# Performance work log

Hardware: AMD Instinct MI355X
Metric: run time of the kernel (lower is better)

## Reference

```python
import jax, jax.numpy as jnp
import numpy as np
from jax import lax

B, N, CIN, COUT, R, K = 4, 16384, 64, 128, 32, 3
VOX_EPS = 1e-6
BN3D_EPS = 1e-4
BN1D_EPS = 1e-5
LRELU_SLOPE = 0.1


def setup_inputs() -> dict:
    key = jax.random.key(0)
    ks = jax.random.split(key, 20)
    d = {}
    d['features'] = jax.random.normal(ks[0], (B, N, CIN), jnp.float32)
    d['coords'] = jax.random.normal(ks[1], (B, N, 3), jnp.float32)
    # Conv3D #1: (D,H,W,Cin,Cout) + bias
    d['conv1_w'] = jax.random.normal(ks[2], (K, K, K, CIN, COUT), jnp.float32) * 0.02
    d['conv1_b'] = jax.random.normal(ks[3], (COUT,), jnp.float32) * 0.02
    d['bn1_g'] = jax.random.uniform(ks[4], (COUT,), jnp.float32, 0.75, 1.25)
    d['bn1_b'] = jax.random.normal(ks[5], (COUT,), jnp.float32) * 0.1
    d['bn1_m'] = jax.random.normal(ks[6], (COUT,), jnp.float32) * 0.1
    d['bn1_v'] = jax.random.uniform(ks[7], (COUT,), jnp.float32, 0.5, 1.5)
    # Conv3D #2
    d['conv2_w'] = jax.random.normal(ks[8], (K, K, K, COUT, COUT), jnp.float32) * 0.02
    d['conv2_b'] = jax.random.normal(ks[9], (COUT,), jnp.float32) * 0.02
    d['bn2_g'] = jax.random.uniform(ks[10], (COUT,), jnp.float32, 0.75, 1.25)
    d['bn2_b'] = jax.random.normal(ks[11], (COUT,), jnp.float32) * 0.1
    d['bn2_m'] = jax.random.normal(ks[12], (COUT,), jnp.float32) * 0.1
    d['bn2_v'] = jax.random.uniform(ks[13], (COUT,), jnp.float32, 0.5, 1.5)
    # Point SharedMLP: Conv1D k=1 -> matmul, + BN + ReLU
    d['pw'] = jax.random.normal(ks[14], (CIN, COUT), jnp.float32) * 0.05
    d['pb'] = jax.random.normal(ks[15], (COUT,), jnp.float32) * 0.02
    d['pbn_g'] = jax.random.uniform(ks[16], (COUT,), jnp.float32, 0.75, 1.25)
    d['pbn_b'] = jax.random.normal(ks[17], (COUT,), jnp.float32) * 0.1
    d['pbn_m'] = jax.random.normal(ks[18], (COUT,), jnp.float32) * 0.1
    d['pbn_v'] = jax.random.uniform(ks[19], (COUT,), jnp.float32, 0.5, 1.5)
    return d


def _bn(x, g, b, m, v, eps):
    return (x - m) * (g * lax.rsqrt(v + eps)) + b


def _leaky_relu(x):
    return jnp.where(x >= 0, x, LRELU_SLOPE * x)


def _pvconv(features, coords, conv1_w, conv1_b, bn1_g, bn1_b, bn1_m, bn1_v,
            conv2_w, conv2_b, bn2_g, bn2_b, bn2_m, bn2_v,
            pw, pb, pbn_g, pbn_b, pbn_m, pbn_v):
    r = R
    # ---- Voxelization (normalize coords, scatter-average into grid) ----
    c = lax.stop_gradient(coords)                                   # (B,N,3)
    nc = c - jnp.mean(c, axis=1, keepdims=True)
    denom = jnp.max(jnp.linalg.norm(nc, axis=2, keepdims=True), axis=1, keepdims=True) * 2.0 + VOX_EPS
    nc = nc / denom + 0.5
    nc = jnp.clip(nc * r, 0.0, r - 1)                                # (B,N,3) in [0, r-1]
    vox = jnp.round(nc).astype(jnp.int32)                            # (B,N,3)

    batch_off = jnp.arange(B, dtype=jnp.int32)[:, None] * (r * r * r)
    lin = batch_off + vox[..., 0] * (r * r) + vox[..., 1] * r + vox[..., 2]  # (B,N)
    lin = lin.reshape(-1)
    feat_flat = features.reshape(-1, CIN)
    sums = jax.ops.segment_sum(feat_flat, lin, num_segments=B * r * r * r)   # (B*r^3,Cin)
    cnts = jax.ops.segment_sum(jnp.ones((B * N,), jnp.float32), lin, num_segments=B * r * r * r)
    cnts = jnp.where(cnts == 0, 1.0, cnts)
    grid = (sums / cnts[:, None]).reshape(B, r, r, r, CIN)           # (B,r,r,r,Cin)

    # ---- Voxel branch: Conv3D -> BN -> LeakyReLU (x2) ----
    dn = ('NDHWC', 'DHWIO', 'NDHWC')
    g = lax.conv_general_dilated(grid, conv1_w, (1, 1, 1), 'SAME', dimension_numbers=dn) + conv1_b
    g = _leaky_relu(_bn(g, bn1_g, bn1_b, bn1_m, bn1_v, BN3D_EPS))
    g = lax.conv_general_dilated(g, conv2_w, (1, 1, 1), 'SAME', dimension_numbers=dn) + conv2_b
    g = _leaky_relu(_bn(g, bn2_g, bn2_b, bn2_m, bn2_v, BN3D_EPS))    # (B,r,r,r,Cout)

    # ---- Trilinear devoxelize: gather 8 corners with interpolation weights ----
    g_flat = g.reshape(B, r * r * r, COUT)
    c0 = jnp.floor(nc).astype(jnp.int32)                             # (B,N,3)
    frac = nc - c0.astype(nc.dtype)
    c1 = jnp.minimum(c0 + 1, r - 1)
    vox_pts = jnp.zeros((B, N, COUT), jnp.float32)
    for dx in (0, 1):
        for dy in (0, 1):
            for dz in (0, 1):
                ix = c1[..., 0] if dx else c0[..., 0]
                iy = c1[..., 1] if dy else c0[..., 1]
                iz = c1[..., 2] if dz else c0[..., 2]
                w = ((frac[..., 0] if dx else 1.0 - frac[..., 0]) *
                     (frac[..., 1] if dy else 1.0 - frac[..., 1]) *
                     (frac[..., 2] if dz else 1.0 - frac[..., 2]))   # (B,N)
                idx = ix * (r * r) + iy * r + iz                      # (B,N)
                gathered = jnp.take_along_axis(g_flat, idx[..., None], axis=1)  # (B,N,Cout)
                vox_pts = vox_pts + w[..., None] * gathered

    # ---- Point branch: SharedMLP (1x1 conv -> BN -> ReLU) ----
    pf = jnp.einsum('bnc,cd->bnd', features, pw) + pb
    pf = jax.nn.relu(_bn(pf, pbn_g, pbn_b, pbn_m, pbn_v, BN1D_EPS))

    return vox_pts + pf                                              # (B,N,Cout)


def reference(features, coords, conv1_w, conv1_b, bn1_g, bn1_b, bn1_m, bn1_v,
              conv2_w, conv2_b, bn2_g, bn2_b, bn2_m, bn2_v,
              pw, pb, pbn_g, pbn_b, pbn_m, pbn_v):
    fused = _pvconv(features, coords, conv1_w, conv1_b, bn1_g, bn1_b, bn1_m, bn1_v,
                    conv2_w, conv2_b, bn2_g, bn2_b, bn2_m, bn2_v,
                    pw, pb, pbn_g, pbn_b, pbn_m, pbn_v)
    return (fused, coords)
```

## Files before the change

kernel.cpp:

```cpp
#include <hip/hip_runtime.h>
#include <hip/hip_bf16.h>

constexpr int B    = 4;
constexpr int N    = 16384;
constexpr int CIN  = 64;
constexpr int COUT = 128;
constexpr int R    = 32;
constexpr int R3   = R * R * R;
constexpr int RP   = 34;
constexpr int RP3  = RP * RP * RP;
constexpr int NVOX = B * R3;
constexpr float VOX_EPS   = 1e-6f;
constexpr float BN3D_EPS  = 1e-4f;
constexpr float BN1D_EPS  = 1e-5f;
constexpr float LRELU     = 0.1f;

typedef __attribute__((ext_vector_type(8))) short bf16x8;
typedef __attribute__((ext_vector_type(4))) float f32x4;
typedef __attribute__((ext_vector_type(8))) unsigned short u16x8;

__device__ inline float bf2f(ushort u) {
    union { unsigned int i; float f; } x; x.i = ((unsigned int)u) << 16; return x.f;
}
__device__ inline ushort f2bf(float f) {
    union { float f; unsigned int i; } x; x.f = f;
    unsigned int r = x.i + 0x7fffu + ((x.i >> 16) & 1u);
    return (ushort)(r >> 16);
}

__device__ inline int swz(int base, int z) {
    return (base ^ (z & 3) ^ ((z >> 2) & 3)) & 3;
}

__global__ __launch_bounds__(256) void k_stats_sum(const float* __restrict__ coords,
                                                   float* __restrict__ stats) {
    int blk = blockIdx.x;
    int b = blk >> 4, stripe = blk & 15;
    const float* c = coords + ((size_t)b * N + stripe * 1024) * 3;
    float sx = 0.f, sy = 0.f, sz = 0.f;
    for (int i = threadIdx.x; i < 1024; i += 256) {
        sx += c[i * 3 + 0];
        sy += c[i * 3 + 1];
        sz += c[i * 3 + 2];
    }
    __shared__ float red[256];
    float vals[3] = {sx, sy, sz};
    for (int k = 0; k < 3; ++k) {
        red[threadIdx.x] = vals[k];
        __syncthreads();
        for (int s = 128; s > 0; s >>= 1) {
            if (threadIdx.x < s) red[threadIdx.x] += red[threadIdx.x + s];
            __syncthreads();
        }
        if (threadIdx.x == 0) atomicAdd(&stats[b * 8 + k], red[0]);
        __syncthreads();
    }
}

__global__ __launch_bounds__(256) void k_stats_max(const float* __restrict__ coords,
                                                   float* __restrict__ stats) {
    int blk = blockIdx.x;
    int b = blk >> 4, stripe = blk & 15;
    const float invN = 1.0f / (float)N;
    float mx = stats[b * 8 + 0] * invN;
    float my = stats[b * 8 + 1] * invN;
    float mz = stats[b * 8 + 2] * invN;
    const float* c = coords + ((size_t)b * N + stripe * 1024) * 3;
    float mm = 0.f;
    for (int i = threadIdx.x; i < 1024; i += 256) {
        float dx = c[i * 3 + 0] - mx;
        float dy = c[i * 3 + 1] - my;
        float dz = c[i * 3 + 2] - mz;
        mm = fmaxf(mm, sqrtf(dx * dx + dy * dy + dz * dz));
    }
    __shared__ float red[256];
    red[threadIdx.x] = mm;
    __syncthreads();
    for (int s = 128; s > 0; s >>= 1) {
        if (threadIdx.x < s) red[threadIdx.x] = fmaxf(red[threadIdx.x], red[threadIdx.x + s]);
        __syncthreads();
    }
    if (threadIdx.x == 0)
        atomicMax((unsigned*)&stats[b * 8 + 3], __float_as_uint(red[0]));
}

__device__ inline void compute_nc(const float* __restrict__ coords,
                                  const float* __restrict__ stats,
                                  int p, int b, float& nx, float& ny, float& nz) {
    const float invN = 1.0f / (float)N;
    float mmax = __uint_as_float(((const unsigned*)stats)[b * 8 + 3]);
    float denom = mmax * 2.0f + VOX_EPS;
    float cx = coords[(size_t)p * 3 + 0];
    float cy = coords[(size_t)p * 3 + 1];
    float cz = coords[(size_t)p * 3 + 2];
    nx = (cx - stats[b * 8 + 0] * invN) / denom + 0.5f;
    ny = (cy - stats[b * 8 + 1] * invN) / denom + 0.5f;
    nz = (cz - stats[b * 8 + 2] * invN) / denom + 0.5f;
    nx = fminf(fmaxf(nx * (float)R, 0.f), (float)(R - 1));
    ny = fminf(fmaxf(ny * (float)R, 0.f), (float)(R - 1));
    nz = fminf(fmaxf(nz * (float)R, 0.f), (float)(R - 1));
}

__global__ __launch_bounds__(256) void k_count(const float* __restrict__ coords,
                                               const float* __restrict__ stats,
                                               int* __restrict__ cnt,
                                               int* __restrict__ plin,
                                               int* __restrict__ pslot) {
    int p = blockIdx.x * 256 + threadIdx.x;
    int b = p >> 14;
    float nx, ny, nz;
    compute_nc(coords, stats, p, b, nx, ny, nz);
    int lin = ((b * R + (int)rintf(nx)) * R + (int)rintf(ny)) * R + (int)rintf(nz);
    plin[p] = lin;
    pslot[p] = atomicAdd(&cnt[lin], 1);
}

__global__ __launch_bounds__(256) void k_scan1(const int* __restrict__ cnt,
                                               int* __restrict__ base,
                                               int* __restrict__ btot) {
    __shared__ int s[256];
    int g = blockIdx.x * 256 + threadIdx.x;
    int val = cnt[g];
    s[threadIdx.x] = val;
    __syncthreads();
    for (int off = 1; off < 256; off <<= 1) {
        int v = threadIdx.x >= off ? s[threadIdx.x - off] : 0;
        __syncthreads();
        s[threadIdx.x] += v;
        __syncthreads();
    }
    base[g] = s[threadIdx.x] - val;
    if (threadIdx.x == 255) btot[blockIdx.x] = s[255];
}

__global__ __launch_bounds__(512) void k_scan2(const int* __restrict__ btot,
                                               int* __restrict__ boff) {
    __shared__ int s[512];
    int val = btot[threadIdx.x];
    s[threadIdx.x] = val;
    __syncthreads();
    for (int off = 1; off < 512; off <<= 1) {
        int v = threadIdx.x >= off ? s[threadIdx.x - off] : 0;
        __syncthreads();
        s[threadIdx.x] += v;
        __syncthreads();
    }
    boff[threadIdx.x] = s[threadIdx.x] - val;
}

__global__ __launch_bounds__(256) void k_fill(const int* __restrict__ plin,
                                              const int* __restrict__ pslot,
                                              const int* __restrict__ base,
                                              const int* __restrict__ boff,
                                              int* __restrict__ order) {
    int p = blockIdx.x * 256 + threadIdx.x;
    int lin = plin[p];
    order[base[lin] + boff[lin >> 8] + pslot[p]] = p;
}

__global__ __launch_bounds__(256) void k_gather(const float* __restrict__ feats,
                                                const int* __restrict__ cnt,
                                                const int* __restrict__ base,
                                                const int* __restrict__ boff,
                                                const int* __restrict__ order,
                                                ushort* __restrict__ gridp) {
    int v = blockIdx.x * 4 + (threadIdx.x >> 6);
    int lane = threadIdx.x & 63;
    int c = cnt[v];
    int bs = base[v] + boff[v >> 8];
    float acc = 0.f;
    for (int j = 0; j < c; ++j) {
        int p = order[bs + j];
        acc += feats[(size_t)p * CIN + lane];
    }
    float val = acc / (float)(c == 0 ? 1 : c);
    int vz = v & 31, vy = (v >> 5) & 31, vx = (v >> 10) & 31, b = v >> 15;
    size_t o = ((((size_t)(b * 2 + (lane >> 5)) * RP + vx + 1) * RP + vy + 1) * RP + (vz + 1)) * 32
               + (lane & 31);
    gridp[o] = f2bf(val);
}

__global__ __launch_bounds__(256) void k_zero_border(ushort* __restrict__ buf, int nchunks) {
    int i = blockIdx.x * 256 + threadIdx.x;
    if (i >= nchunks) return;
    int v = i >> 2;
    int r = v % RP3;
    int z = r % RP;
    int t = r / RP;
    int y = t % RP;
    int x = (t / RP) % RP;
    if (x == 0 || x == RP - 1 || y == 0 || y == RP - 1 || z == 0 || z == RP - 1)
        *(uint4*)(buf + (size_t)i * 8) = make_uint4(0u, 0u, 0u, 0u);
}

__global__ __launch_bounds__(256) void k_wq_all(const float* __restrict__ w1,
                                                const float* __restrict__ w2,
                                                const float* __restrict__ pw,
                                                ushort* __restrict__ wq) {
    int idx = blockIdx.x * 256 + threadIdx.x;
    int g = idx >> 12;
    const float* src; int gl;
    if (g < 54)       { src = w1; gl = g; }
    else if (g < 162) { src = w2; gl = g - 54; }
    else              { src = pw; gl = g - 162; }
    int j    = idx & 7;
    int lane = (idx >> 3) & 63;
    int nt   = (idx >> 9) & 7;
    int k = gl * 32 + ((lane >> 4) << 3) + j;
    int n = nt * 16 + (lane & 15);
    wq[idx] = f2bf(src[(size_t)k * COUT + n]);
}

template <int CI, bool PLANAR_OUT>
__global__ __launch_bounds__(256, 3) void k_conv_mfma(const ushort* __restrict__ in,
                                                      const ushort* __restrict__ wq,
                                                      const float* __restrict__ bias,
                                                      const float* __restrict__ bng,
                                                      const float* __restrict__ bnb,
                                                      const float* __restrict__ bnm,
                                                      const float* __restrict__ bnv,
                                                      ushort* __restrict__ out) {
    constexpr int NCHI = CI / 32;
    __shared__ __align__(16) ushort sl[18 * RP * 32];

    int bid = blockIdx.x;
    int Y = bid & 7;
    int x = (bid >> 3) & 31;
    int b = bid >> 8;
    int y0 = Y * 4;
    int tid = threadIdx.x;
    int wave = tid >> 6, lane = tid & 63, quad = lane >> 4, l16 = lane & 15;
    int wm = wave >> 1, wn = wave & 1;

    f32x4 acc[4][4] = {};

    for (int cc = 0; cc < NCHI; ++cc) {
        const ushort* base = in + (((size_t)(b * NCHI + cc) * RP + x) * RP + y0) * RP * 32;
        __syncthreads();
        for (int t = tid; t < 18 * 136; t += 256) {
            int row = t / 136;
            int r   = t - row * 136;
            int X = row / 6, Yl = row - X * 6;
            uint4 v = *(const uint4*)(base + ((size_t)(X * RP + Yl) * RP) * 32 + r * 8);
            int z = r >> 2, ch = r & 3;
            *(uint4*)(sl + ((row * RP + z) * 4 + swz(ch, z)) * 8) = v;
        }
        __syncthreads();

        for (int tap = 0; tap < 27; ++tap) {
            int dx = tap / 9, rem = tap - dx * 9;
            int dy = rem / 3, dz = rem - dy * 3;

            const ushort* bp = wq + ((size_t)((tap * NCHI + cc) * 8 + wn * 4) * 64 + lane) * 8;
            bf16x8 bfr[4], afr[4];
#pragma unroll
            for (int nt = 0; nt < 4; ++nt)
                bfr[nt] = *(const bf16x8*)(bp + nt * 512);
#pragma unroll
            for (int mt = 0; mt < 4; ++mt) {
                int row18 = dx * 6 + wm * 2 + (mt >> 1) + dy;
                int zrow = ((mt & 1) << 4) + l16 + dz;
                afr[mt] = *(const bf16x8*)(sl + ((row18 * RP + zrow) * 4 + swz(quad, zrow)) * 8);
            }
#pragma unroll
            for (int mt = 0; mt < 4; ++mt)
#pragma unroll
                for (int nt = 0; nt < 4; ++nt)
                    acc[mt][nt] = __builtin_amdgcn_mfma_f32_16x16x32_bf16(
                        afr[mt], bfr[nt], acc[mt][nt], 0, 0, 0);
        }
    }

    float sc[4], sb[4], bs[4];
#pragma unroll
    for (int nt = 0; nt < 4; ++nt) {
        int co = wn * 64 + nt * 16 + l16;
        sc[nt] = bng[co] * rsqrtf(bnv[co] + BN3D_EPS);
        sb[nt] = bnb[co] - bnm[co] * sc[nt];
        bs[nt] = bias[co];
    }
#pragma unroll
    for (int mt = 0; mt < 4; ++mt) {
#pragma unroll
        for (int reg = 0; reg < 4; ++reg) {
            int m = wm * 64 + mt * 16 + quad * 4 + reg;
            int i = m >> 5, z = m & 31;
#pragma unroll
            for (int nt = 0; nt < 4; ++nt) {
                float v = (acc[mt][nt][reg] + bs[nt]) * sc[nt] + sb[nt];
                v = v >= 0.f ? v : LRELU * v;
                int co = wn * 64 + nt * 16 + l16;
                if (PLANAR_OUT) {
                    size_t o = ((((size_t)(b * 4 + (co >> 5)) * RP + (x + 1)) * RP
                                 + (y0 + i + 1)) * RP + (z + 1)) * 32 + (co & 31);
                    out[o] = f2bf(v);
                } else {
                    size_t o = (((size_t)(b * R + x) * R + (y0 + i)) * R + z) * COUT + co;
                    out[o] = f2bf(v);
                }
            }
        }
    }
}

__global__ __launch_bounds__(256, 2) void k_devox(const float* __restrict__ coords,
                                                  const float* __restrict__ feats,
                                                  const float* __restrict__ stats,
                                                  const ushort* __restrict__ g2,
                                                  const ushort* __restrict__ pwq,
                                                  const float* __restrict__ pb,
                                                  const float* __restrict__ pg,
                                                  const float* __restrict__ pbb,
                                                  const float* __restrict__ pm,
                                                  const float* __restrict__ pv,
                                                  float* __restrict__ out) {
    __shared__ __align__(16) ushort sfeat[128 * 64];
    __shared__ __align__(16) ushort smlp[128 * 128];
    __shared__ int   sidx[128 * 8];
    __shared__ float swt[128 * 8];

    int blk = blockIdx.x, tid = threadIdx.x;
    int wave = tid >> 6, lane = tid & 63, quad = lane >> 4, l16 = lane & 15;
    int p0 = blk * 128;

    if (tid < 128) {
        int p = p0 + tid, b = p >> 14;
        float nx, ny, nz;
        compute_nc(coords, stats, p, b, nx, ny, nz);
        int cx0 = (int)floorf(nx), cy0 = (int)floorf(ny), cz0 = (int)floorf(nz);
        float fx = nx - (float)cx0, fy = ny - (float)cy0, fz = nz - (float)cz0;
        int cx1 = min(cx0 + 1, R - 1), cy1 = min(cy0 + 1, R - 1), cz1 = min(cz0 + 1, R - 1);
#pragma unroll
        for (int k = 0; k < 8; ++k) {
            int dx = (k >> 2) & 1, dy = (k >> 1) & 1, dz = k & 1;
            int ix = dx ? cx1 : cx0;
            int iy = dy ? cy1 : cy0;
            int iz = dz ? cz1 : cz0;
            sidx[tid * 8 + k] = (((b * R + ix) * R + iy) * R + iz) * COUT;
            swt[tid * 8 + k] = (dx ? fx : 1.f - fx) * (dy ? fy : 1.f - fy) * (dz ? fz : 1.f - fz);
        }
    }
    for (int i = 0; i < 4; ++i) {
        int c = i * 256 + tid;
        int p = c >> 3, ch = c & 7;
        const float* src = feats + (size_t)(p0 + p) * CIN + ch * 8;
        float4 f0 = *(const float4*)src;
        float4 f1 = *(const float4*)(src + 4);
        u16x8 u;
        u[0] = f2bf(f0.x); u[1] = f2bf(f0.y); u[2] = f2bf(f0.z); u[3] = f2bf(f0.w);
        u[4] = f2bf(f1.x); u[5] = f2bf(f1.y); u[6] = f2bf(f1.z); u[7] = f2bf(f1.w);
        *(u16x8*)&sfeat[(p * 8 + (ch ^ (p & 7))) * 8] = u;
    }
    __syncthreads();

    f32x4 acc[8][2] = {};
#pragma unroll
    for (int cc = 0; cc < 2; ++cc) {
        const ushort* bp = pwq + ((size_t)(cc * 8 + wave * 2) * 64 + lane) * 8;
        bf16x8 b0 = *(const bf16x8*)bp;
        bf16x8 b1 = *(const bf16x8*)(bp + 512);
#pragma unroll
        for (int mt = 0; mt < 8; ++mt) {
            int prow = mt * 16 + l16;
            int ch = cc * 4 + quad;
            bf16x8 a = *(const bf16x8*)&sfeat[(prow * 8 + (ch ^ (prow & 7))) * 8];
            acc[mt][0] = __builtin_amdgcn_mfma_f32_16x16x32_bf16(a, b0, acc[mt][0], 0, 0, 0);
            acc[mt][1] = __builtin_amdgcn_mfma_f32_16x16x32_bf16(a, b1, acc[mt][1], 0, 0, 0);
        }
    }

    int co0 = wave * 32 + l16, co1 = co0 + 16;
    {
        float sc0 = pg[co0] * rsqrtf(pv[co0] + BN1D_EPS);
        float sb0 = pbb[co0] - pm[co0] * sc0;
        float bs0 = pb[co0];
        float sc1 = pg[co1] * rsqrtf(pv[co1] + BN1D_EPS);
        float sb1 = pbb[co1] - pm[co1] * sc1;
        float bs1 = pb[co1];
#pragma unroll
        for (int mt = 0; mt < 8; ++mt) {
#pragma unroll
            for (int reg = 0; reg < 4; ++reg) {
                int pl = mt * 16 + quad * 4 + reg;
                smlp[pl * 128 + co0] = f2bf(fmaxf((acc[mt][0][reg] + bs0) * sc0 + sb0, 0.f));
                smlp[pl * 128 + co1] = f2bf(fmaxf((acc[mt][1][reg] + bs1) * sc1 + sb1, 0.f));
            }
        }
    }
    __syncthreads();

#pragma unroll
    for (int it = 0; it < 8; ++it) {
        int t = it * 256 + tid;
        int p = t >> 4, c = t & 15;
        float a[8];
        const ushort* m = &smlp[p * 128 + c * 8];
#pragma unroll
        for (int j = 0; j < 8; ++j) a[j] = bf2f(m[j]);
#pragma unroll
        for (int k = 0; k < 8; ++k) {
            int idx = sidx[p * 8 + k];
            float w = swt[p * 8 + k];
            bf16x8 row = *(const bf16x8*)(g2 + (size_t)idx + c * 8);
#pragma unroll
            for (int j = 0; j < 8; ++j) a[j] += w * bf2f(((u16x8)row)[j]);
        }
        float* o = out + (size_t)(p0 + p) * COUT + c * 8;
        *(float4*)o       = make_float4(a[0], a[1], a[2], a[3]);
        *(float4*)(o + 4) = make_float4(a[4], a[5], a[6], a[7]);
    }
}

extern "C" void kernel_launch(void* const* d_in, const int* in_sizes, int n_in,
                              void* d_out, int out_size, void* d_ws, size_t ws_size,
                              hipStream_t stream) {
    const float* feats   = (const float*)d_in[0];
    const float* coords  = (const float*)d_in[1];
    const float* conv1_w = (const float*)d_in[2];
    const float* conv1_b = (const float*)d_in[3];
    const float* bn1_g   = (const float*)d_in[4];
    const float* bn1_b   = (const float*)d_in[5];
    const float* bn1_m   = (const float*)d_in[6];
    const float* bn1_v   = (const float*)d_in[7];
    const float* conv2_w = (const float*)d_in[8];
    const float* conv2_b = (const float*)d_in[9];
    const float* bn2_g   = (const float*)d_in[10];
    const float* bn2_b   = (const float*)d_in[11];
    const float* bn2_m   = (const float*)d_in[12];
    const float* bn2_v   = (const float*)d_in[13];
    const float* pw      = (const float*)d_in[14];
    const float* pb      = (const float*)d_in[15];
    const float* pbn_g   = (const float*)d_in[16];
    const float* pbn_b   = (const float*)d_in[17];
    const float* pbn_m   = (const float*)d_in[18];
    const float* pbn_v   = (const float*)d_in[19];

    char* p = (char*)d_ws;
    float* stats = (float*)p;                        p += 256;
    int*   cnt   = (int*)p;                          p += (size_t)NVOX * 4;
    int*   plin  = (int*)p;                          p += (size_t)B * N * 4;
    int*   pslot = (int*)p;                          p += (size_t)B * N * 4;
    int*   base  = (int*)p;                          p += (size_t)NVOX * 4;
    int*   btot  = (int*)p;                          p += 512 * 4;
    int*   boff  = (int*)p;                          p += 512 * 4;
    int*   order = (int*)p;                          p += (size_t)B * N * 4;
    ushort* gridp = (ushort*)p;                      p += (size_t)B * 2 * RP3 * 32 * 2;
    ushort* g1p   = (ushort*)p;                      p += (size_t)B * 4 * RP3 * 32 * 2;
    ushort* g2b   = (ushort*)p;                      p += (size_t)B * R3 * COUT * 2;
    ushort* wq    = (ushort*)p;                      p += (size_t)164 * 4096 * 2;
    ushort* wq1 = wq;
    ushort* wq2 = wq + 54 * 4096;
    ushort* pwq = wq + 162 * 4096;
    float*  outf  = (float*)d_out;

    hipMemsetAsync(stats, 0, 256 + (size_t)NVOX * 4, stream);
    {
        int nc = B * 6 * RP3 * 4;
        k_zero_border<<<(nc + 255) / 256, 256, 0, stream>>>(gridp, nc);
    }

    k_stats_sum<<<64, 256, 0, stream>>>(coords, stats);
    k_stats_max<<<64, 256, 0, stream>>>(coords, stats);

    k_count<<<(B * N) / 256, 256, 0, stream>>>(coords, stats, cnt, plin, pslot);
    k_scan1<<<NVOX / 256, 256, 0, stream>>>(cnt, base, btot);
    k_scan2<<<1, 512, 0, stream>>>(btot, boff);
    k_fill<<<(B * N) / 256, 256, 0, stream>>>(plin, pslot, base, boff, order);
    k_gather<<<NVOX / 4, 256, 0, stream>>>(feats, cnt, base, boff, order, gridp);

    k_wq_all<<<(164 * 4096) / 256, 256, 0, stream>>>(conv1_w, conv2_w, pw, wq);

    k_conv_mfma<CIN, true><<<B * R * (R / 4), 256, 0, stream>>>(
        gridp, wq1, conv1_b, bn1_g, bn1_b, bn1_m, bn1_v, g1p);
    k_conv_mfma<COUT, false><<<B * R * (R / 4), 256, 0, stream>>>(
        g1p, wq2, conv2_b, bn2_g, bn2_b, bn2_m, bn2_v, g2b);

    k_devox<<<(B * N) / 128, 256, 0, stream>>>(coords, feats, stats, g2b, pwq, pb,
                                               pbn_g, pbn_b, pbn_m, pbn_v, outf);

    hipMemcpyAsync(outf + (size_t)B * N * COUT, coords, (size_t)B * N * 3 * sizeof(float),
                   hipMemcpyDeviceToDevice, stream);
}
```

Before: 354.1 us.

## Fuse voxelization preprocessing into one persistent kernel with grid barriers

Merges the stats, count, scan, fill, gather, border-zeroing and weight-quantization kernels into a single 256-block persistent kernel that uses atomic grid-wide barriers between phases. The coords copy moves from a separate memcpy into the tail of the devox kernel. This removes about ten kernel launches and their gaps. In exchange the gather phase now runs on only 256 blocks instead of 8192, which lowers parallelism. The spin barriers also assume all blocks are co-resident.

```diff
diff --git a/kernel.cpp b/kernel.cpp
--- a/kernel.cpp
+++ b/kernel.cpp
@@ -32,56 +32,15 @@
     return (base ^ (z & 3) ^ ((z >> 2) & 3)) & 3;
 }
 
-__global__ __launch_bounds__(256) void k_stats_sum(const float* __restrict__ coords,
-                                                   float* __restrict__ stats) {
-    int blk = blockIdx.x;
-    int b = blk >> 4, stripe = blk & 15;
-    const float* c = coords + ((size_t)b * N + stripe * 1024) * 3;
-    float sx = 0.f, sy = 0.f, sz = 0.f;
-    for (int i = threadIdx.x; i < 1024; i += 256) {
-        sx += c[i * 3 + 0];
-        sy += c[i * 3 + 1];
-        sz += c[i * 3 + 2];
-    }
-    __shared__ float red[256];
-    float vals[3] = {sx, sy, sz};
-    for (int k = 0; k < 3; ++k) {
-        red[threadIdx.x] = vals[k];
-        __syncthreads();
-        for (int s = 128; s > 0; s >>= 1) {
-            if (threadIdx.x < s) red[threadIdx.x] += red[threadIdx.x + s];
-            __syncthreads();
-        }
-        if (threadIdx.x == 0) atomicAdd(&stats[b * 8 + k], red[0]);
-        __syncthreads();
-    }
-}
-
-__global__ __launch_bounds__(256) void k_stats_max(const float* __restrict__ coords,
-                                                   float* __restrict__ stats) {
-    int blk = blockIdx.x;
-    int b = blk >> 4, stripe = blk & 15;
-    const float invN = 1.0f / (float)N;
-    float mx = stats[b * 8 + 0] * invN;
-    float my = stats[b * 8 + 1] * invN;
-    float mz = stats[b * 8 + 2] * invN;
-    const float* c = coords + ((size_t)b * N + stripe * 1024) * 3;
-    float mm = 0.f;
-    for (int i = threadIdx.x; i < 1024; i += 256) {
-        float dx = c[i * 3 + 0] - mx;
-        float dy = c[i * 3 + 1] - my;
-        float dz = c[i * 3 + 2] - mz;
-        mm = fmaxf(mm, sqrtf(dx * dx + dy * dy + dz * dz));
-    }
-    __shared__ float red[256];
-    red[threadIdx.x] = mm;
+__device__ inline void gridbar(int* bar, int idx, int nblk) {
     __syncthreads();
-    for (int s = 128; s > 0; s >>= 1) {
-        if (threadIdx.x < s) red[threadIdx.x] = fmaxf(red[threadIdx.x], red[threadIdx.x + s]);
-        __syncthreads();
-    }
-    if (threadIdx.x == 0)
-        atomicMax((unsigned*)&stats[b * 8 + 3], __float_as_uint(red[0]));
+    if (threadIdx.x == 0) {
+        __hip_atomic_fetch_add(&bar[idx], 1, __ATOMIC_ACQ_REL, __HIP_MEMORY_SCOPE_AGENT);
+        while (__hip_atomic_load(&bar[idx], __ATOMIC_ACQUIRE, __HIP_MEMORY_SCOPE_AGENT) < nblk) {
+            __builtin_amdgcn_s_sleep(1);
+        }
+    }
+    __syncthreads();
 }
 
 __device__ inline void compute_nc(const float* __restrict__ coords,
@@ -101,114 +60,176 @@
     nz = fminf(fmaxf(nz * (float)R, 0.f), (float)(R - 1));
 }
 
-__global__ __launch_bounds__(256) void k_count(const float* __restrict__ coords,
-                                               const float* __restrict__ stats,
-                                               int* __restrict__ cnt,
-                                               int* __restrict__ plin,
-                                               int* __restrict__ pslot) {
-    int p = blockIdx.x * 256 + threadIdx.x;
-    int b = p >> 14;
-    float nx, ny, nz;
-    compute_nc(coords, stats, p, b, nx, ny, nz);
-    int lin = ((b * R + (int)rintf(nx)) * R + (int)rintf(ny)) * R + (int)rintf(nz);
-    plin[p] = lin;
-    pslot[p] = atomicAdd(&cnt[lin], 1);
-}
-
-__global__ __launch_bounds__(256) void k_scan1(const int* __restrict__ cnt,
-                                               int* __restrict__ base,
-                                               int* __restrict__ btot) {
-    __shared__ int s[256];
-    int g = blockIdx.x * 256 + threadIdx.x;
-    int val = cnt[g];
-    s[threadIdx.x] = val;
-    __syncthreads();
-    for (int off = 1; off < 256; off <<= 1) {
-        int v = threadIdx.x >= off ? s[threadIdx.x - off] : 0;
-        __syncthreads();
-        s[threadIdx.x] += v;
-        __syncthreads();
-    }
-    base[g] = s[threadIdx.x] - val;
-    if (threadIdx.x == 255) btot[blockIdx.x] = s[255];
-}
-
-__global__ __launch_bounds__(512) void k_scan2(const int* __restrict__ btot,
-                                               int* __restrict__ boff) {
+__global__ __launch_bounds__(256) void k_pre(const float* __restrict__ coords,
+                                             const float* __restrict__ feats,
+                                             const float* __restrict__ w1,
+                                             const float* __restrict__ w2,
+                                             const float* __restrict__ pw,
+                                             float* __restrict__ stats,
+                                             int* __restrict__ bar,
+                                             int* __restrict__ cnt,
+                                             int* __restrict__ plin,
+                                             int* __restrict__ pslot,
+                                             int* __restrict__ base,
+                                             int* __restrict__ btot,
+                                             int* __restrict__ boff,
+                                             int* __restrict__ order,
+                                             ushort* __restrict__ wq,
+                                             ushort* __restrict__ gridp) {
+    int tid = threadIdx.x, blk = blockIdx.x;
+    int gtid = blk * 256 + tid;
     __shared__ int s[512];
-    int val = btot[threadIdx.x];
-    s[threadIdx.x] = val;
-    __syncthreads();
-    for (int off = 1; off < 512; off <<= 1) {
-        int v = threadIdx.x >= off ? s[threadIdx.x - off] : 0;
-        __syncthreads();
-        s[threadIdx.x] += v;
-        __syncthreads();
-    }
-    boff[threadIdx.x] = s[threadIdx.x] - val;
-}
-
-__global__ __launch_bounds__(256) void k_fill(const int* __restrict__ plin,
-                                              const int* __restrict__ pslot,
-                                              const int* __restrict__ base,
-                                              const int* __restrict__ boff,
-                                              int* __restrict__ order) {
-    int p = blockIdx.x * 256 + threadIdx.x;
-    int lin = plin[p];
-    order[base[lin] + boff[lin >> 8] + pslot[p]] = p;
-}
-
-__global__ __launch_bounds__(256) void k_gather(const float* __restrict__ feats,
-                                                const int* __restrict__ cnt,
-                                                const int* __restrict__ base,
-                                                const int* __restrict__ boff,
-                                                const int* __restrict__ order,
-                                                ushort* __restrict__ gridp) {
-    int v = blockIdx.x * 4 + (threadIdx.x >> 6);
-    int lane = threadIdx.x & 63;
-    int c = cnt[v];
-    int bs = base[v] + boff[v >> 8];
-    float acc = 0.f;
-    for (int j = 0; j < c; ++j) {
-        int p = order[bs + j];
-        acc += feats[(size_t)p * CIN + lane];
-    }
-    float val = acc / (float)(c == 0 ? 1 : c);
-    int vz = v & 31, vy = (v >> 5) & 31, vx = (v >> 10) & 31, b = v >> 15;
-    size_t o = ((((size_t)(b * 2 + (lane >> 5)) * RP + vx + 1) * RP + vy + 1) * RP + (vz + 1)) * 32
-               + (lane & 31);
-    gridp[o] = f2bf(val);
-}
-
-__global__ __launch_bounds__(256) void k_zero_border(ushort* __restrict__ buf, int nchunks) {
-    int i = blockIdx.x * 256 + threadIdx.x;
-    if (i >= nchunks) return;
-    int v = i >> 2;
-    int r = v % RP3;
-    int z = r % RP;
-    int t = r / RP;
-    int y = t % RP;
-    int x = (t / RP) % RP;
-    if (x == 0 || x == RP - 1 || y == 0 || y == RP - 1 || z == 0 || z == RP - 1)
-        *(uint4*)(buf + (size_t)i * 8) = make_uint4(0u, 0u, 0u, 0u);
-}
-
-__global__ __launch_bounds__(256) void k_wq_all(const float* __restrict__ w1,
-                                                const float* __restrict__ w2,
-                                                const float* __restrict__ pw,
-                                                ushort* __restrict__ wq) {
-    int idx = blockIdx.x * 256 + threadIdx.x;
-    int g = idx >> 12;
-    const float* src; int gl;
-    if (g < 54)       { src = w1; gl = g; }
-    else if (g < 162) { src = w2; gl = g - 54; }
-    else              { src = pw; gl = g - 162; }
-    int j    = idx & 7;
-    int lane = (idx >> 3) & 63;
-    int nt   = (idx >> 9) & 7;
-    int k = gl * 32 + ((lane >> 4) << 3) + j;
-    int n = nt * 16 + (lane & 15);
-    wq[idx] = f2bf(src[(size_t)k * COUT + n]);
+    __shared__ float red[256];
+
+    cnt[gtid] = 0;
+    cnt[gtid + 65536] = 0;
+    for (int i = gtid; i < 24 * RP3 * 4; i += 65536) {
+        int v = i >> 2;
+        int r = v % RP3;
+        int z = r % RP;
+        int t2 = r / RP;
+        int y = t2 % RP;
+        int x = (t2 / RP) % RP;
+        if (x == 0 || x == RP - 1 || y == 0 || y == RP - 1 || z == 0 || z == RP - 1)
+            *(uint4*)(gridp + (size_t)i * 8) = make_uint4(0u, 0u, 0u, 0u);
+    }
+    for (int idx = gtid; idx < 164 * 4096; idx += 65536) {
+        int g = idx >> 12;
+        const float* src; int gl;
+        if (g < 54)       { src = w1; gl = g; }
+        else if (g < 162) { src = w2; gl = g - 54; }
+        else              { src = pw; gl = g - 162; }
+        int j    = idx & 7;
+        int lane = (idx >> 3) & 63;
+        int nt   = (idx >> 9) & 7;
+        int k = gl * 32 + ((lane >> 4) << 3) + j;
+        int n = nt * 16 + (lane & 15);
+        wq[idx] = f2bf(src[(size_t)k * COUT + n]);
+    }
+
+    if (blk < 64) {
+        int b = blk >> 4, stripe = blk & 15;
+        const float* c = coords + ((size_t)b * N + stripe * 1024) * 3;
+        float sx = 0.f, sy = 0.f, sz = 0.f;
+        for (int i = tid; i < 1024; i += 256) {
+            sx += c[i * 3 + 0];
+            sy += c[i * 3 + 1];
+            sz += c[i * 3 + 2];
+        }
+        float vals[3] = {sx, sy, sz};
+        for (int k = 0; k < 3; ++k) {
+            red[tid] = vals[k];
+            __syncthreads();
+            for (int st = 128; st > 0; st >>= 1) {
+                if (tid < st) red[tid] += red[tid + st];
+                __syncthreads();
+            }
+            if (tid == 0) atomicAdd(&stats[b * 8 + k], red[0]);
+            __syncthreads();
+        }
+    }
+    gridbar(bar, 0, 256);
+
+    if (blk < 64) {
+        int b = blk >> 4, stripe = blk & 15;
+        const float invN = 1.0f / (float)N;
+        float mx = stats[b * 8 + 0] * invN;
+        float my = stats[b * 8 + 1] * invN;
+        float mz = stats[b * 8 + 2] * invN;
+        const float* c = coords + ((size_t)b * N + stripe * 1024) * 3;
+        float mm = 0.f;
+        for (int i = tid; i < 1024; i += 256) {
+            float dx = c[i * 3 + 0] - mx;
+            float dy = c[i * 3 + 1] - my;
+            float dz = c[i * 3 + 2] - mz;
+            mm = fmaxf(mm, sqrtf(dx * dx + dy * dy + dz * dz));
+        }
+        red[tid] = mm;
+        __syncthreads();
+        for (int st = 128; st > 0; st >>= 1) {
+            if (tid < st) red[tid] = fmaxf(red[tid], red[tid + st]);
+            __syncthreads();
+        }
+        if (tid == 0)
+            atomicMax((unsigned*)&stats[b * 8 + 3], __float_as_uint(red[0]));
+    }
+    gridbar(bar, 1, 256);
+
+    {
+        int p = gtid, b = p >> 14;
+        float nx, ny, nz;
+        compute_nc(coords, stats, p, b, nx, ny, nz);
+        int lin = ((b * R + (int)rintf(nx)) * R + (int)rintf(ny)) * R + (int)rintf(nz);
+        plin[p] = lin;
+        pslot[p] = atomicAdd(&cnt[lin], 1);
+    }
+    gridbar(bar, 2, 256);
+
+    for (int cch = blk * 2; cch <= blk * 2 + 1; ++cch) {
+        int g = cch * 256 + tid;
+        int val = cnt[g];
+        s[tid] = val;
+        __syncthreads();
+        for (int off = 1; off < 256; off <<= 1) {
+            int v = tid >= off ? s[tid - off] : 0;
+            __syncthreads();
+            s[tid] += v;
+            __syncthreads();
+        }
+        base[g] = s[tid] - val;
+        if (tid == 255) btot[cch] = s[255];
+        __syncthreads();
+    }
+    gridbar(bar, 3, 256);
+
+    if (blk == 0) {
+        int v0 = btot[tid], v1 = btot[tid + 256];
+        s[tid] = v0; s[tid + 256] = v1;
+        __syncthreads();
+        for (int off = 1; off < 256; off <<= 1) {
+            int v = tid >= off ? s[tid - off] : 0;
+            __syncthreads();
+            s[tid] += v;
+            __syncthreads();
+        }
+        int half = s[255];
+        __syncthreads();
+        for (int off = 1; off < 256; off <<= 1) {
+            int v = tid >= off ? s[256 + tid - off] : 0;
+            __syncthreads();
+            s[256 + tid] += v;
+            __syncthreads();
+        }
+        boff[tid] = s[tid] - v0;
+        boff[tid + 256] = s[256 + tid] - v1 + half;
+    }
+    gridbar(bar, 4, 256);
+
+    {
+        int p = gtid;
+        int lin = plin[p];
+        order[base[lin] + boff[lin >> 8] + pslot[p]] = p;
+    }
+    gridbar(bar, 5, 256);
+
+    {
+        int wid = blk * 4 + (tid >> 6);
+        int lane = tid & 63;
+        for (int v = wid; v < NVOX; v += 1024) {
+            int c = cnt[v];
+            int bs = base[v] + boff[v >> 8];
+            float acc = 0.f;
+            for (int j = 0; j < c; ++j) {
+                int p = order[bs + j];
+                acc += feats[(size_t)p * CIN + lane];
+            }
+            float val = acc / (float)(c == 0 ? 1 : c);
+            int vz = v & 31, vy = (v >> 5) & 31, vx = (v >> 10) & 31, b = v >> 15;
+            size_t o = ((((size_t)(b * 2 + (lane >> 5)) * RP + vx + 1) * RP + vy + 1) * RP
+                        + (vz + 1)) * 32 + (lane & 31);
+            gridp[o] = f2bf(val);
+        }
+    }
 }
 
 template <int CI, bool PLANAR_OUT>
@@ -408,6 +429,12 @@
         float* o = out + (size_t)(p0 + p) * COUT + c * 8;
         *(float4*)o       = make_float4(a[0], a[1], a[2], a[3]);
         *(float4*)(o + 4) = make_float4(a[4], a[5], a[6], a[7]);
+    }
+
+    {
+        float* dst = out + (size_t)B * N * COUT;
+        for (int i = blk * 256 + tid; i < B * N * 3; i += 512 * 256)
+            dst[i] = coords[i];
     }
 }
 
@@ -437,6 +464,7 @@
 
     char* p = (char*)d_ws;
     float* stats = (float*)p;                        p += 256;
+    int*   bar   = (int*)p;                          p += 256;
     int*   cnt   = (int*)p;                          p += (size_t)NVOX * 4;
     int*   plin  = (int*)p;                          p += (size_t)B * N * 4;
     int*   pslot = (int*)p;                          p += (size_t)B * N * 4;
@@ -453,22 +481,11 @@
     ushort* pwq = wq + 162 * 4096;
     float*  outf  = (float*)d_out;
 
-    hipMemsetAsync(stats, 0, 256 + (size_t)NVOX * 4, stream);
-    {
-        int nc = B * 6 * RP3 * 4;
-        k_zero_border<<<(nc + 255) / 256, 256, 0, stream>>>(gridp, nc);
-    }
-
-    k_stats_sum<<<64, 256, 0, stream>>>(coords, stats);
-    k_stats_max<<<64, 256, 0, stream>>>(coords, stats);
-
-    k_count<<<(B * N) / 256, 256, 0, stream>>>(coords, stats, cnt, plin, pslot);
-    k_scan1<<<NVOX / 256, 256, 0, stream>>>(cnt, base, btot);
-    k_scan2<<<1, 512, 0, stream>>>(btot, boff);
-    k_fill<<<(B * N) / 256, 256, 0, stream>>>(plin, pslot, base, boff, order);
-    k_gather<<<NVOX / 4, 256, 0, stream>>>(feats, cnt, base, boff, order, gridp);
-
-    k_wq_all<<<(164 * 4096) / 256, 256, 0, stream>>>(conv1_w, conv2_w, pw, wq);
+    hipMemsetAsync(stats, 0, 512, stream);
+
+    k_pre<<<256, 256, 0, stream>>>(coords, feats, conv1_w, conv2_w, pw,
+                                   stats, bar, cnt, plin, pslot, base, btot, boff,
+                                   order, wq, gridp);
 
     k_conv_mfma<CIN, true><<<B * R * (R / 4), 256, 0, stream>>>(
         gridp, wq1, conv1_b, bn1_g, bn1_b, bn1_m, bn1_v, g1p);
@@ -477,7 +494,4 @@
 
     k_devox<<<(B * N) / 128, 256, 0, stream>>>(coords, feats, stats, g2b, pwq, pb,
                                                pbn_g, pbn_b, pbn_m, pbn_v, outf);
-
-    hipMemcpyAsync(outf + (size_t)B * N * COUT, coords, (size_t)B * N * 3 * sizeof(float),
-                   hipMemcpyDeviceToDevice, stream);
-}
+}
```

Result: slower. 870.8 us (+146.0%).
